# Optimization experiments

Measured on AMD Instinct MI355X. Metric: run time of the kernel, lower is better.

Reference implementation:

```python
import jax, jax.numpy as jnp
import numpy as np

NUM_HEADS = 16
NUM_KV_HEADS = 4
HEAD_DIM = 128
ROPE_THETA = 500000.0
RMS_EPS = 1e-5


def _rms_norm(x, w, eps=RMS_EPS):
    # normalize over last dim in fp32, as in YuaRMSNorm
    xf = x.astype(jnp.float32)
    var = jnp.mean(xf * xf, axis=-1, keepdims=True)
    return (w * (xf * jax.lax.rsqrt(var + eps))).astype(x.dtype)


def _rotate_half(x):
    x1, x2 = jnp.split(x, 2, axis=-1)
    return jnp.concatenate([-x2, x1], axis=-1)


def _rope_cos_sin(seq_len, dim, dtype):
    inv_freq = 1.0 / (ROPE_THETA ** (jnp.arange(0, dim, 2, dtype=jnp.float32) / dim))
    pos = jnp.arange(seq_len, dtype=jnp.float32)
    freqs = pos[:, None] * inv_freq[None, :]          # [S, dim/2]
    emb = jnp.concatenate([freqs, freqs], axis=-1)     # [S, dim]
    return jnp.cos(emb).astype(dtype), jnp.sin(emb).astype(dtype)


def setup_inputs() -> dict:
    key = jax.random.key(0)
    ks = jax.random.split(key, 5)
    B, S, H = 2, 2048, 2048
    q_out = NUM_HEADS * HEAD_DIM
    kv_out = NUM_KV_HEADS * HEAD_DIM
    sc = 0.02
    return {
        "hidden_states": jax.random.normal(ks[0], (B, S, H), jnp.float32),
        "q_w": jax.random.normal(ks[1], (q_out, H), jnp.float32) * sc,
        "k_w": jax.random.normal(ks[2], (kv_out, H), jnp.float32) * sc,
        "v_w": jax.random.normal(ks[3], (kv_out, H), jnp.float32) * sc,
        "o_w": jax.random.normal(ks[4], (H, q_out), jnp.float32) * sc,
        "q_norm_w": jnp.ones((HEAD_DIM,), jnp.float32),
        "k_norm_w": jnp.ones((HEAD_DIM,), jnp.float32),
    }


def reference(hidden_states, q_w, k_w, v_w, o_w, q_norm_w, k_norm_w):
    B, S, H = hidden_states.shape
    groups = NUM_HEADS // NUM_KV_HEADS

    # fused-ish QKV projections (torch Linear: x @ W^T)
    q = jnp.einsum('bsh,oh->bso', hidden_states, q_w).reshape(B, S, NUM_HEADS, HEAD_DIM).transpose(0, 2, 1, 3)
    k = jnp.einsum('bsh,oh->bso', hidden_states, k_w).reshape(B, S, NUM_KV_HEADS, HEAD_DIM).transpose(0, 2, 1, 3)
    v = jnp.einsum('bsh,oh->bso', hidden_states, v_w).reshape(B, S, NUM_KV_HEADS, HEAD_DIM).transpose(0, 2, 1, 3)

    # QK RMSNorm over head_dim
    q = _rms_norm(q, q_norm_w)
    k = _rms_norm(k, k_norm_w)

    # RoPE (position_ids = arange(S))
    cos, sin = _rope_cos_sin(S, HEAD_DIM, q.dtype)  # [S, hd]
    cos = cos[None, None]  # [1,1,S,hd]
    sin = sin[None, None]
    q = q * cos + _rotate_half(q) * sin
    k = k * cos + _rotate_half(k) * sin

    # GQA repeat_interleave of kv heads
    k = jnp.repeat(k, groups, axis=1)  # [B, num_heads, S, hd]
    v = jnp.repeat(v, groups, axis=1)

    # causal SDPA
    scale = 1.0 / jnp.sqrt(jnp.asarray(HEAD_DIM, q.dtype))
    scores = jnp.einsum('bhqd,bhkd->bhqk', q, k) * scale
    causal = jnp.tril(jnp.ones((S, S), bool))
    scores = jnp.where(causal[None, None], scores, jnp.finfo(scores.dtype).min)
    probs = jax.nn.softmax(scores, axis=-1)
    attn = jnp.einsum('bhqk,bhkd->bhqd', probs, v)

    attn = attn.transpose(0, 2, 1, 3).reshape(B, S, NUM_HEADS * HEAD_DIM)
    return jnp.einsum('bso,ho->bsh', attn, o_w)
```

## Files before the change

kernel.cpp:

```cpp
#include <hip/hip_runtime.h>
#include <stdint.h>

#define S_LEN 2048
#define BATCH 2
#define NH 16
#define NKV 4
#define HD 128
#define HID 2048
#define MROWS (BATCH * S_LEN)
#define PST 72

typedef unsigned short u16;
typedef __attribute__((ext_vector_type(8))) short frag_ab;
typedef __attribute__((ext_vector_type(4))) float frag_cd;

static __device__ __forceinline__ float bf2f(u16 v) {
    union { unsigned u; float f; } t; t.u = ((unsigned)v) << 16; return t.f;
}
static __device__ __forceinline__ u16 f2bf(float f) {
    union { float f; unsigned u; } t; t.f = f;
    unsigned r = t.u + 0x7fffu + ((t.u >> 16) & 1u);
    return (u16)(r >> 16);
}
static __device__ __forceinline__ void load_lds16(const u16* g, u16* l) {
    __builtin_amdgcn_global_load_lds((const __attribute__((address_space(1))) void*)g,
                                     (__attribute__((address_space(3))) void*)l, 16, 0, 0);
}

__global__ __launch_bounds__(256) void conv_f32_bf16(const float* __restrict__ src,
                                                     u16* __restrict__ dst, int n4) {
    int i = blockIdx.x * 256 + threadIdx.x;
    if (i >= n4) return;
    float4 v = ((const float4*)src)[i];
    ushort4 o;
    o.x = f2bf(v.x); o.y = f2bf(v.y); o.z = f2bf(v.z); o.w = f2bf(v.w);
    ((ushort4*)dst)[i] = o;
}

__global__ __launch_bounds__(256) void gemm_bt(const u16* __restrict__ A, const u16* __restrict__ B,
                                               float* __restrict__ C, int M, int N, int K) {
    __shared__ u16 As[128 * 32];
    __shared__ u16 Bs[128 * 32];
    const int tid = threadIdx.x;
    const int wave = tid >> 6, lane = tid & 63;
    const int quad = lane >> 4, lr = lane & 15;
    const int wm = (wave & 1) * 64, wn = (wave >> 1) * 64;
    const long bm = (long)blockIdx.x * 128, bn = (long)blockIdx.y * 128;
    const int srow = (wave << 4) + (lane >> 2);
    const int scol = (lane & 3) * 8;
    const u16* Ag = A + (bm + srow) * (long)K + scol;
    const u16* Bg = B + (bn + srow) * (long)K + scol;
    u16* AsW = As + wave * 512;
    u16* BsW = Bs + wave * 512;

    frag_cd acc[4][4];
#pragma unroll
    for (int i = 0; i < 4; i++)
#pragma unroll
        for (int j = 0; j < 4; j++) acc[i][j] = (frag_cd){0.f, 0.f, 0.f, 0.f};

    for (int k0 = 0; k0 < K; k0 += 32) {
        __syncthreads();
        load_lds16(Ag + k0, AsW);
        load_lds16(Ag + (long)64 * K + k0, AsW + 2048);
        load_lds16(Bg + k0, BsW);
        load_lds16(Bg + (long)64 * K + k0, BsW + 2048);
        __syncthreads();
        frag_ab af[4], bfr[4];
#pragma unroll
        for (int i = 0; i < 4; i++) af[i] = *(const frag_ab*)(As + (wm + i * 16 + lr) * 32 + quad * 8);
#pragma unroll
        for (int j = 0; j < 4; j++) bfr[j] = *(const frag_ab*)(Bs + (wn + j * 16 + lr) * 32 + quad * 8);
#pragma unroll
        for (int i = 0; i < 4; i++)
#pragma unroll
            for (int j = 0; j < 4; j++)
                acc[i][j] = __builtin_amdgcn_mfma_f32_16x16x32_bf16(af[i], bfr[j], acc[i][j], 0, 0, 0);
    }
#pragma unroll
    for (int i = 0; i < 4; i++)
#pragma unroll
        for (int j = 0; j < 4; j++)
#pragma unroll
            for (int r = 0; r < 4; r++) {
                long row = bm + wm + i * 16 + quad * 4 + r;
                long col = bn + wn + j * 16 + lr;
                C[row * N + col] = acc[i][j][r];
            }
}

__global__ __launch_bounds__(256) void gemm_bt64(const u16* __restrict__ A, const u16* __restrict__ B,
                                                 float* __restrict__ C, int M, int N, int K) {
    __shared__ u16 As[128 * 32];
    __shared__ u16 Bs[64 * 32];
    const int tid = threadIdx.x;
    const int wave = tid >> 6, lane = tid & 63;
    const int quad = lane >> 4, lr = lane & 15;
    const int wm = (wave & 1) * 64, wn = (wave >> 1) * 32;
    const long bm = (long)blockIdx.x * 128, bn = (long)blockIdx.y * 64;
    const int srow = (wave << 4) + (lane >> 2);
    const int scol = (lane & 3) * 8;
    const u16* Ag = A + (bm + srow) * (long)K + scol;
    const u16* Bg = B + (bn + srow) * (long)K + scol;
    u16* AsW = As + wave * 512;
    u16* BsW = Bs + wave * 512;

    frag_cd acc[4][2];
#pragma unroll
    for (int i = 0; i < 4; i++)
#pragma unroll
        for (int j = 0; j < 2; j++) acc[i][j] = (frag_cd){0.f, 0.f, 0.f, 0.f};

    for (int k0 = 0; k0 < K; k0 += 32) {
        __syncthreads();
        load_lds16(Ag + k0, AsW);
        load_lds16(Ag + (long)64 * K + k0, AsW + 2048);
        load_lds16(Bg + k0, BsW);
        __syncthreads();
        frag_ab af[4], bfr[2];
#pragma unroll
        for (int i = 0; i < 4; i++) af[i] = *(const frag_ab*)(As + (wm + i * 16 + lr) * 32 + quad * 8);
#pragma unroll
        for (int j = 0; j < 2; j++) bfr[j] = *(const frag_ab*)(Bs + (wn + j * 16 + lr) * 32 + quad * 8);
#pragma unroll
        for (int i = 0; i < 4; i++)
#pragma unroll
            for (int j = 0; j < 2; j++)
                acc[i][j] = __builtin_amdgcn_mfma_f32_16x16x32_bf16(af[i], bfr[j], acc[i][j], 0, 0, 0);
    }
#pragma unroll
    for (int i = 0; i < 4; i++)
#pragma unroll
        for (int j = 0; j < 2; j++)
#pragma unroll
            for (int r = 0; r < 4; r++) {
                long row = bm + wm + i * 16 + quad * 4 + r;
                long col = bn + wn + j * 16 + lr;
                C[row * N + col] = acc[i][j][r];
            }
}

__global__ __launch_bounds__(256) void rope_norm(const float* __restrict__ src, u16* __restrict__ dst,
                                                 const float* __restrict__ nw, int nh, int stride, int coff) {
    const int m = blockIdx.x;
    const int wave = threadIdx.x >> 6, lane = threadIdx.x & 63;
    const int s = m & (S_LEN - 1), b = m >> 11;
    const int d0 = 2 * lane;
    const float w0 = nw[d0], w1 = nw[d0 + 1];
    const int i0 = d0 & 63;
    const float lnt_over = 13.122363377404328f / 64.f;
    float inv0 = expf(-(float)i0 * lnt_over);
    float inv1 = expf(-(float)(i0 + 1) * lnt_over);
    float c0 = cosf((float)s * inv0), sn0 = sinf((float)s * inv0);
    float c1 = cosf((float)s * inv1), sn1 = sinf((float)s * inv1);
    for (int h = wave; h < nh; h += 4) {
        float2 x = *(const float2*)(src + (long)m * stride + coff + h * HD + d0);
        float ss = x.x * x.x + x.y * x.y;
#pragma unroll
        for (int off = 1; off < 64; off <<= 1) ss += __shfl_xor(ss, off);
        float rs = rsqrtf(ss * (1.f / HD) + 1e-5f);
        float xn0 = x.x * rs * w0;
        float xn1 = x.y * rs * w1;
        float p0 = __shfl_xor(xn0, 32);
        float p1 = __shfl_xor(xn1, 32);
        float r0 = (lane < 32) ? -p0 : p0;
        float r1 = (lane < 32) ? -p1 : p1;
        float y0 = xn0 * c0 + r0 * sn0;
        float y1 = xn1 * c1 + r1 * sn1;
        unsigned outw = (unsigned)f2bf(y0) | ((unsigned)f2bf(y1) << 16);
        *(unsigned*)(dst + (((long)(b * nh + h) * S_LEN + s) * HD + d0)) = outw;
    }
}

__global__ __launch_bounds__(256) void pack_vt(const float* __restrict__ src, u16* __restrict__ dst,
                                               int stride, int coff) {
    __shared__ u16 t[128 * 72];
    const int tid = threadIdx.x;
    const int st = blockIdx.x & 31;
    const int kh = (blockIdx.x >> 5) & 3;
    const int b = blockIdx.x >> 7;
    const long m0 = (long)b * S_LEN + st * 64;
#pragma unroll
    for (int c = 0; c < 8; c++) {
        int idx = c * 256 + tid;
        int r = idx >> 5, cg = idx & 31;
        float4 v = *(const float4*)(src + (m0 + r) * stride + coff + kh * HD + cg * 4);
        int col = cg * 4;
        t[(col + 0) * 72 + r] = f2bf(v.x);
        t[(col + 1) * 72 + r] = f2bf(v.y);
        t[(col + 2) * 72 + r] = f2bf(v.z);
        t[(col + 3) * 72 + r] = f2bf(v.w);
    }
    __syncthreads();
    const int d = tid >> 1, sh = (tid & 1) * 32;
    u16* dp = dst + ((long)(b * NKV + kh) * HD + d) * S_LEN + st * 64 + sh;
    const u16* tp = &t[d * 72 + sh];
    *(uint4*)(dp + 0)  = *(const uint4*)(tp + 0);
    *(uint4*)(dp + 8)  = *(const uint4*)(tp + 8);
    *(uint4*)(dp + 16) = *(const uint4*)(tp + 16);
    *(uint4*)(dp + 24) = *(const uint4*)(tp + 24);
}

__global__ __launch_bounds__(256, 2) void flash_attn(const u16* __restrict__ Q, const u16* __restrict__ K,
                                                     const u16* __restrict__ Vt, u16* __restrict__ O) {
    __shared__ __align__(16) char shmem[19456];
    u16* Pls = (u16*)shmem;
    float* maccf = (float*)shmem;
    float* mlbf = (float*)(shmem + 18432);
#define MACC(mt, dt, c, r) (((((mt) * 8 + (dt)) * 16 + (c)) * 16) + (r))
#define MLB(w, mt, row, j) (((((w) * 2 + (mt)) * 16 + (row)) * 2) + (j))
    const int tid = threadIdx.x;
    const int wave = tid >> 6, lane = tid & 63;
    const int quad = lane >> 4, lr = lane & 15;
    const int g = blockIdx.x & 7;
    const int sub = (blockIdx.x >> 3) & 3;
    const int tt = blockIdx.x >> 5;
    const int t = 63 - tt;
    const int b = g >> 2, kh = g & 3;
    const int h = kh * 4 + sub;
    const float scale = 0.08838834764831845f;
    const u16* Qb = Q + ((long)(b * NH + h) * S_LEN) * HD;
    const u16* Kb = K + ((long)(b * NKV + kh) * S_LEN) * HD;
    const u16* Vb = Vt + ((long)(b * NKV + kh) * HD) * S_LEN;
    const int pbase = wave * 32 * PST;

    const int q0 = t * 32;
    const int nkt = (t >> 1) + 1;

    frag_ab qf[2][4];
#pragma unroll
    for (int mt = 0; mt < 2; mt++) {
        int qrow = q0 + mt * 16 + lr;
#pragma unroll
        for (int ks = 0; ks < 4; ks++)
            qf[mt][ks] = *(const frag_ab*)(Qb + (long)qrow * HD + ks * 32 + quad * 8);
    }
    frag_cd oa[2][8];
    float m_i[2][4], l_i[2][4];
#pragma unroll
    for (int mt = 0; mt < 2; mt++) {
#pragma unroll
        for (int dt = 0; dt < 8; dt++) oa[mt][dt] = (frag_cd){0.f, 0.f, 0.f, 0.f};
#pragma unroll
        for (int r = 0; r < 4; r++) { m_i[mt][r] = -3e38f; l_i[mt][r] = 0.f; }
    }

    for (int kt = wave; kt < nkt; kt += 4) {
        const int j0 = kt * 64;
        frag_cd sa[2][4];
#pragma unroll
        for (int mt = 0; mt < 2; mt++)
#pragma unroll
            for (int nt = 0; nt < 4; nt++) sa[mt][nt] = (frag_cd){0.f, 0.f, 0.f, 0.f};
#pragma unroll
        for (int nt = 0; nt < 4; nt++) {
            frag_ab kf[4];
#pragma unroll
            for (int ks = 0; ks < 4; ks++)
                kf[ks] = *(const frag_ab*)(Kb + (long)(j0 + nt * 16 + lr) * HD + ks * 32 + quad * 8);
#pragma unroll
            for (int mt = 0; mt < 2; mt++)
#pragma unroll
                for (int ks = 0; ks < 4; ks++)
                    sa[mt][nt] = __builtin_amdgcn_mfma_f32_16x16x32_bf16(qf[mt][ks], kf[ks], sa[mt][nt], 0, 0, 0);
        }
        frag_ab vf[2][8];
#pragma unroll
        for (int ks = 0; ks < 2; ks++)
#pragma unroll
            for (int dt = 0; dt < 8; dt++)
                vf[ks][dt] = *(const frag_ab*)(Vb + (long)(dt * 16 + lr) * S_LEN + j0 + ks * 32 + quad * 8);

        const bool need_mask = (j0 + 63) > q0;
#pragma unroll
        for (int mt = 0; mt < 2; mt++) {
            float mrow[4] = {-3e38f, -3e38f, -3e38f, -3e38f};
#pragma unroll
            for (int nt = 0; nt < 4; nt++) {
                int key = j0 + nt * 16 + lr;
#pragma unroll
                for (int r = 0; r < 4; r++) {
                    int qrow = q0 + mt * 16 + quad * 4 + r;
                    float v = sa[mt][nt][r] * scale;
                    if (need_mask) v = (key <= qrow) ? v : -3e38f;
                    sa[mt][nt][r] = v;
                    mrow[r] = fmaxf(mrow[r], v);
                }
            }
#pragma unroll
            for (int off = 1; off < 16; off <<= 1)
#pragma unroll
                for (int r = 0; r < 4; r++) mrow[r] = fmaxf(mrow[r], __shfl_xor(mrow[r], off));
            float rs[4];
#pragma unroll
            for (int r = 0; r < 4; r++) {
                float mn = fmaxf(m_i[mt][r], mrow[r]);
                float alpha = __expf(m_i[mt][r] - mn);
                m_i[mt][r] = mn;
                l_i[mt][r] *= alpha;
                rs[r] = 0.f;
#pragma unroll
                for (int dt = 0; dt < 8; dt++) oa[mt][dt][r] *= alpha;
            }
#pragma unroll
            for (int nt = 0; nt < 4; nt++)
#pragma unroll
                for (int r = 0; r < 4; r++) {
                    float pw = __expf(sa[mt][nt][r] - m_i[mt][r]);
                    rs[r] += pw;
                    Pls[pbase + (mt * 16 + quad * 4 + r) * PST + nt * 16 + lr] = f2bf(pw);
                }
#pragma unroll
            for (int off = 1; off < 16; off <<= 1)
#pragma unroll
                for (int r = 0; r < 4; r++) rs[r] += __shfl_xor(rs[r], off);
#pragma unroll
            for (int r = 0; r < 4; r++) l_i[mt][r] += rs[r];
        }

#pragma unroll
        for (int ks = 0; ks < 2; ks++) {
            frag_ab pf[2];
#pragma unroll
            for (int mt = 0; mt < 2; mt++)
                pf[mt] = *(const frag_ab*)&Pls[pbase + (mt * 16 + lr) * PST + ks * 32 + quad * 8];
#pragma unroll
            for (int dt = 0; dt < 8; dt++) {
                oa[0][dt] = __builtin_amdgcn_mfma_f32_16x16x32_bf16(pf[0], vf[ks][dt], oa[0][dt], 0, 0, 0);
                oa[1][dt] = __builtin_amdgcn_mfma_f32_16x16x32_bf16(pf[1], vf[ks][dt], oa[1][dt], 0, 0, 0);
            }
        }
    }

    if (lr == 0) {
#pragma unroll
        for (int mt = 0; mt < 2; mt++)
#pragma unroll
            for (int r = 0; r < 4; r++) {
                mlbf[MLB(wave, mt, quad * 4 + r, 0)] = m_i[mt][r];
                mlbf[MLB(wave, mt, quad * 4 + r, 1)] = l_i[mt][r];
            }
    }
    __syncthreads();
    float inv[2][4];
#pragma unroll
    for (int mt = 0; mt < 2; mt++)
#pragma unroll
        for (int r = 0; r < 4; r++) {
            int row = quad * 4 + r;
            float m0 = mlbf[MLB(0, mt, row, 0)], m1 = mlbf[MLB(1, mt, row, 0)];
            float m2 = mlbf[MLB(2, mt, row, 0)], m3 = mlbf[MLB(3, mt, row, 0)];
            float ms = fmaxf(fmaxf(m0, m1), fmaxf(m2, m3));
            float ls = mlbf[MLB(0, mt, row, 1)] * __expf(m0 - ms) + mlbf[MLB(1, mt, row, 1)] * __expf(m1 - ms)
                     + mlbf[MLB(2, mt, row, 1)] * __expf(m2 - ms) + mlbf[MLB(3, mt, row, 1)] * __expf(m3 - ms);
            inv[mt][r] = 1.f / ls;
            float alpha = __expf(m_i[mt][r] - ms);
#pragma unroll
            for (int dt = 0; dt < 8; dt++) oa[mt][dt][r] *= alpha;
        }
    for (int w = 0; w < 4; w++) {
        if (wave == w) {
#pragma unroll
            for (int mt = 0; mt < 2; mt++)
#pragma unroll
                for (int dt = 0; dt < 8; dt++) {
                    frag_cd* pp = (frag_cd*)&maccf[MACC(mt, dt, lr, quad * 4)];
                    if (w == 0) *pp = oa[mt][dt];
                    else {
                        frag_cd o = *pp;
#pragma unroll
                        for (int r = 0; r < 4; r++) o[r] += oa[mt][dt][r];
                        *pp = o;
                    }
                }
        }
        __syncthreads();
    }
#pragma unroll
    for (int mt = 0; mt < 2; mt++)
#pragma unroll
        for (int dto = 0; dto < 2; dto++) {
            int dt = wave * 2 + dto;
            frag_cd v = *(const frag_cd*)&maccf[MACC(mt, dt, lr, quad * 4)];
#pragma unroll
            for (int r = 0; r < 4; r++) {
                int s = q0 + mt * 16 + quad * 4 + r;
                O[((long)b * S_LEN + s) * (NH * HD) + h * HD + dt * 16 + lr] =
                    f2bf(v[r] * inv[mt][r]);
            }
        }
#undef MACC
#undef MLB
}

extern "C" void kernel_launch(void* const* d_in, const int* in_sizes, int n_in,
                              void* d_out, int out_size, void* d_ws, size_t ws_size,
                              hipStream_t stream) {
    const float* hs  = (const float*)d_in[0];
    const float* q_w = (const float*)d_in[1];
    const float* k_w = (const float*)d_in[2];
    const float* v_w = (const float*)d_in[3];
    const float* o_w = (const float*)d_in[4];
    const float* qnw = (const float*)d_in[5];
    const float* knw = (const float*)d_in[6];
    float* out = (float*)d_out;
    char* ws = (char*)d_ws;
    (void)in_sizes; (void)n_in; (void)out_size;

    if (ws_size >= (100ul << 20)) {
        u16* hs_bf  = (u16*)(ws);
        u16* wbuf   = (u16*)(ws + (16ul << 20));
        float* gout = (float*)(ws + (28ul << 20));
        u16* Kr     = (u16*)(ws + (76ul << 20));
        u16* Vt     = (u16*)(ws + (80ul << 20));
        u16* Qr     = (u16*)(ws + (84ul << 20));
        const int NQKV = HID + 2 * NKV * HD;

        conv_f32_bf16<<<(MROWS * HID / 4 + 255) / 256, 256, 0, stream>>>(hs, hs_bf, MROWS * HID / 4);
        conv_f32_bf16<<<(HID * HID / 4 + 255) / 256, 256, 0, stream>>>(q_w, wbuf, HID * HID / 4);
        conv_f32_bf16<<<(NKV * HD * HID / 4 + 255) / 256, 256, 0, stream>>>(k_w, wbuf + (long)HID * HID, NKV * HD * HID / 4);
        conv_f32_bf16<<<(NKV * HD * HID / 4 + 255) / 256, 256, 0, stream>>>(v_w, wbuf + (long)(HID + NKV * HD) * HID, NKV * HD * HID / 4);

        dim3 gqkv(MROWS / 128, NQKV / 128);
        gemm_bt<<<gqkv, 256, 0, stream>>>(hs_bf, wbuf, gout, MROWS, NQKV, HID);

        rope_norm<<<MROWS, 256, 0, stream>>>(gout, Qr, qnw, NH, NQKV, 0);
        rope_norm<<<MROWS, 256, 0, stream>>>(gout, Kr, knw, NKV, NQKV, HID);
        pack_vt<<<BATCH * NKV * (S_LEN / 64), 256, 0, stream>>>(gout, Vt, NQKV, HID + NKV * HD);

        flash_attn<<<2048, 256, 0, stream>>>(Qr, Kr, Vt, hs_bf);

        conv_f32_bf16<<<(HID * HID / 4 + 255) / 256, 256, 0, stream>>>(o_w, wbuf, HID * HID / 4);
        dim3 go(MROWS / 128, HID / 64);
        gemm_bt64<<<go, 256, 0, stream>>>(hs_bf, wbuf, out, MROWS, HID, HID);
    } else {
        u16* hs_bf  = (u16*)(ws);
        u16* wbuf   = (u16*)(ws + (16ul << 20));
        float* gout = (float*)(ws + (24ul << 20));
        u16* Kr     = (u16*)(ws + (40ul << 20));
        u16* Vt     = (u16*)(ws + (44ul << 20));
        u16* Qr     = (u16*)(ws + (56ul << 20));

        conv_f32_bf16<<<(MROWS * HID / 4 + 255) / 256, 256, 0, stream>>>(hs, hs_bf, MROWS * HID / 4);

        conv_f32_bf16<<<(HID * HID / 4 + 255) / 256, 256, 0, stream>>>(q_w, wbuf, HID * HID / 4);
        dim3 gq(MROWS / 128, HID / 128);
        gemm_bt<<<gq, 256, 0, stream>>>(hs_bf, wbuf, gout, MROWS, HID, HID);
        rope_norm<<<MROWS, 256, 0, stream>>>(gout, Qr, qnw, NH, HID, 0);

        conv_f32_bf16<<<(NKV * HD * HID / 4 + 255) / 256, 256, 0, stream>>>(k_w, wbuf, NKV * HD * HID / 4);
        conv_f32_bf16<<<(NKV * HD * HID / 4 + 255) / 256, 256, 0, stream>>>(v_w, wbuf + NKV * HD * HID, NKV * HD * HID / 4);
        dim3 gkv(MROWS / 128, (2 * NKV * HD) / 64);
        gemm_bt64<<<gkv, 256, 0, stream>>>(hs_bf, wbuf, gout, MROWS, 2 * NKV * HD, HID);
        rope_norm<<<MROWS, 256, 0, stream>>>(gout, Kr, knw, NKV, 2 * NKV * HD, 0);
        pack_vt<<<BATCH * NKV * (S_LEN / 64), 256, 0, stream>>>(gout, Vt, 2 * NKV * HD, NKV * HD);

        flash_attn<<<2048, 256, 0, stream>>>(Qr, Kr, Vt, hs_bf);

        conv_f32_bf16<<<(HID * HID / 4 + 255) / 256, 256, 0, stream>>>(o_w, wbuf, HID * HID / 4);
        dim3 go(MROWS / 128, HID / 64);
        gemm_bt64<<<go, 256, 0, stream>>>(hs_bf, wbuf, out, MROWS, HID, HID);
    }
}
```

Baseline: 423.2 us.

## Split KV projection along K into two GEMMs and sum in fused norm/pack

Drops the large-workspace fused QKV path and always uses separate projections. The Q GEMM moves to the 128x64 tile kernel, which gives more blocks. The small KV GEMM is split along the reduction dimension into two launches using new lda/ldb stride parameters, which doubles the block count for better CU occupancy. The partial results are summed inside new rope_norm_sum and pack_vt_sum kernels. Kr and Vt now alias the weight buffer region, and the change adds an extra fp32 partial buffer plus additional reads.

```diff
diff --git a/kernel.cpp b/kernel.cpp
--- a/kernel.cpp
+++ b/kernel.cpp
@@ -90,7 +90,8 @@
 }
 
 __global__ __launch_bounds__(256) void gemm_bt64(const u16* __restrict__ A, const u16* __restrict__ B,
-                                                 float* __restrict__ C, int M, int N, int K) {
+                                                 float* __restrict__ C, int M, int N, int K,
+                                                 int lda, int ldb) {
     __shared__ u16 As[128 * 32];
     __shared__ u16 Bs[64 * 32];
     const int tid = threadIdx.x;
@@ -100,8 +101,8 @@
     const long bm = (long)blockIdx.x * 128, bn = (long)blockIdx.y * 64;
     const int srow = (wave << 4) + (lane >> 2);
     const int scol = (lane & 3) * 8;
-    const u16* Ag = A + (bm + srow) * (long)K + scol;
-    const u16* Bg = B + (bn + srow) * (long)K + scol;
+    const u16* Ag = A + (bm + srow) * (long)lda + scol;
+    const u16* Bg = B + (bn + srow) * (long)ldb + scol;
     u16* AsW = As + wave * 512;
     u16* BsW = Bs + wave * 512;
 
@@ -114,7 +115,7 @@
     for (int k0 = 0; k0 < K; k0 += 32) {
         __syncthreads();
         load_lds16(Ag + k0, AsW);
-        load_lds16(Ag + (long)64 * K + k0, AsW + 2048);
+        load_lds16(Ag + (long)64 * lda + k0, AsW + 2048);
         load_lds16(Bg + k0, BsW);
         __syncthreads();
         frag_ab af[4], bfr[2];
@@ -172,6 +173,41 @@
     }
 }
 
+__global__ __launch_bounds__(256) void rope_norm_sum(const float* __restrict__ src1, const float* __restrict__ src2,
+                                                     u16* __restrict__ dst, const float* __restrict__ nw,
+                                                     int nh, int stride, int coff) {
+    const int m = blockIdx.x;
+    const int wave = threadIdx.x >> 6, lane = threadIdx.x & 63;
+    const int s = m & (S_LEN - 1), b = m >> 11;
+    const int d0 = 2 * lane;
+    const float w0 = nw[d0], w1 = nw[d0 + 1];
+    const int i0 = d0 & 63;
+    const float lnt_over = 13.122363377404328f / 64.f;
+    float inv0 = expf(-(float)i0 * lnt_over);
+    float inv1 = expf(-(float)(i0 + 1) * lnt_over);
+    float c0 = cosf((float)s * inv0), sn0 = sinf((float)s * inv0);
+    float c1 = cosf((float)s * inv1), sn1 = sinf((float)s * inv1);
+    for (int h = wave; h < nh; h += 4) {
+        float2 x1 = *(const float2*)(src1 + (long)m * stride + coff + h * HD + d0);
+        float2 x2 = *(const float2*)(src2 + (long)m * stride + coff + h * HD + d0);
+        float2 x; x.x = x1.x + x2.x; x.y = x1.y + x2.y;
+        float ss = x.x * x.x + x.y * x.y;
+#pragma unroll
+        for (int off = 1; off < 64; off <<= 1) ss += __shfl_xor(ss, off);
+        float rs = rsqrtf(ss * (1.f / HD) + 1e-5f);
+        float xn0 = x.x * rs * w0;
+        float xn1 = x.y * rs * w1;
+        float p0 = __shfl_xor(xn0, 32);
+        float p1 = __shfl_xor(xn1, 32);
+        float r0 = (lane < 32) ? -p0 : p0;
+        float r1 = (lane < 32) ? -p1 : p1;
+        float y0 = xn0 * c0 + r0 * sn0;
+        float y1 = xn1 * c1 + r1 * sn1;
+        unsigned outw = (unsigned)f2bf(y0) | ((unsigned)f2bf(y1) << 16);
+        *(unsigned*)(dst + (((long)(b * nh + h) * S_LEN + s) * HD + d0)) = outw;
+    }
+}
+
 __global__ __launch_bounds__(256) void pack_vt(const float* __restrict__ src, u16* __restrict__ dst,
                                                int stride, int coff) {
     __shared__ u16 t[128 * 72];
@@ -185,6 +221,38 @@
         int idx = c * 256 + tid;
         int r = idx >> 5, cg = idx & 31;
         float4 v = *(const float4*)(src + (m0 + r) * stride + coff + kh * HD + cg * 4);
+        int col = cg * 4;
+        t[(col + 0) * 72 + r] = f2bf(v.x);
+        t[(col + 1) * 72 + r] = f2bf(v.y);
+        t[(col + 2) * 72 + r] = f2bf(v.z);
+        t[(col + 3) * 72 + r] = f2bf(v.w);
+    }
+    __syncthreads();
+    const int d = tid >> 1, sh = (tid & 1) * 32;
+    u16* dp = dst + ((long)(b * NKV + kh) * HD + d) * S_LEN + st * 64 + sh;
+    const u16* tp = &t[d * 72 + sh];
+    *(uint4*)(dp + 0)  = *(const uint4*)(tp + 0);
+    *(uint4*)(dp + 8)  = *(const uint4*)(tp + 8);
+    *(uint4*)(dp + 16) = *(const uint4*)(tp + 16);
+    *(uint4*)(dp + 24) = *(const uint4*)(tp + 24);
+}
+
+__global__ __launch_bounds__(256) void pack_vt_sum(const float* __restrict__ src1, const float* __restrict__ src2,
+                                                   u16* __restrict__ dst, int stride, int coff) {
+    __shared__ u16 t[128 * 72];
+    const int tid = threadIdx.x;
+    const int st = blockIdx.x & 31;
+    const int kh = (blockIdx.x >> 5) & 3;
+    const int b = blockIdx.x >> 7;
+    const long m0 = (long)b * S_LEN + st * 64;
+#pragma unroll
+    for (int c = 0; c < 8; c++) {
+        int idx = c * 256 + tid;
+        int r = idx >> 5, cg = idx & 31;
+        long off = (m0 + r) * stride + coff + kh * HD + cg * 4;
+        float4 v1 = *(const float4*)(src1 + off);
+        float4 v2 = *(const float4*)(src2 + off);
+        float4 v; v.x = v1.x + v2.x; v.y = v1.y + v2.y; v.z = v1.z + v2.z; v.w = v1.w + v2.w;
         int col = cg * 4;
         t[(col + 0) * 72 + r] = f2bf(v.x);
         t[(col + 1) * 72 + r] = f2bf(v.y);
@@ -405,60 +473,33 @@
     const float* knw = (const float*)d_in[6];
     float* out = (float*)d_out;
     char* ws = (char*)d_ws;
-    (void)in_sizes; (void)n_in; (void)out_size;
-
-    if (ws_size >= (100ul << 20)) {
-        u16* hs_bf  = (u16*)(ws);
-        u16* wbuf   = (u16*)(ws + (16ul << 20));
-        float* gout = (float*)(ws + (28ul << 20));
-        u16* Kr     = (u16*)(ws + (76ul << 20));
-        u16* Vt     = (u16*)(ws + (80ul << 20));
-        u16* Qr     = (u16*)(ws + (84ul << 20));
-        const int NQKV = HID + 2 * NKV * HD;
-
-        conv_f32_bf16<<<(MROWS * HID / 4 + 255) / 256, 256, 0, stream>>>(hs, hs_bf, MROWS * HID / 4);
-        conv_f32_bf16<<<(HID * HID / 4 + 255) / 256, 256, 0, stream>>>(q_w, wbuf, HID * HID / 4);
-        conv_f32_bf16<<<(NKV * HD * HID / 4 + 255) / 256, 256, 0, stream>>>(k_w, wbuf + (long)HID * HID, NKV * HD * HID / 4);
-        conv_f32_bf16<<<(NKV * HD * HID / 4 + 255) / 256, 256, 0, stream>>>(v_w, wbuf + (long)(HID + NKV * HD) * HID, NKV * HD * HID / 4);
-
-        dim3 gqkv(MROWS / 128, NQKV / 128);
-        gemm_bt<<<gqkv, 256, 0, stream>>>(hs_bf, wbuf, gout, MROWS, NQKV, HID);
-
-        rope_norm<<<MROWS, 256, 0, stream>>>(gout, Qr, qnw, NH, NQKV, 0);
-        rope_norm<<<MROWS, 256, 0, stream>>>(gout, Kr, knw, NKV, NQKV, HID);
-        pack_vt<<<BATCH * NKV * (S_LEN / 64), 256, 0, stream>>>(gout, Vt, NQKV, HID + NKV * HD);
-
-        flash_attn<<<2048, 256, 0, stream>>>(Qr, Kr, Vt, hs_bf);
-
-        conv_f32_bf16<<<(HID * HID / 4 + 255) / 256, 256, 0, stream>>>(o_w, wbuf, HID * HID / 4);
-        dim3 go(MROWS / 128, HID / 64);
-        gemm_bt64<<<go, 256, 0, stream>>>(hs_bf, wbuf, out, MROWS, HID, HID);
-    } else {
-        u16* hs_bf  = (u16*)(ws);
-        u16* wbuf   = (u16*)(ws + (16ul << 20));
-        float* gout = (float*)(ws + (24ul << 20));
-        u16* Kr     = (u16*)(ws + (40ul << 20));
-        u16* Vt     = (u16*)(ws + (44ul << 20));
-        u16* Qr     = (u16*)(ws + (56ul << 20));
-
-        conv_f32_bf16<<<(MROWS * HID / 4 + 255) / 256, 256, 0, stream>>>(hs, hs_bf, MROWS * HID / 4);
-
-        conv_f32_bf16<<<(HID * HID / 4 + 255) / 256, 256, 0, stream>>>(q_w, wbuf, HID * HID / 4);
-        dim3 gq(MROWS / 128, HID / 128);
-        gemm_bt<<<gq, 256, 0, stream>>>(hs_bf, wbuf, gout, MROWS, HID, HID);
-        rope_norm<<<MROWS, 256, 0, stream>>>(gout, Qr, qnw, NH, HID, 0);
-
-        conv_f32_bf16<<<(NKV * HD * HID / 4 + 255) / 256, 256, 0, stream>>>(k_w, wbuf, NKV * HD * HID / 4);
-        conv_f32_bf16<<<(NKV * HD * HID / 4 + 255) / 256, 256, 0, stream>>>(v_w, wbuf + NKV * HD * HID, NKV * HD * HID / 4);
-        dim3 gkv(MROWS / 128, (2 * NKV * HD) / 64);
-        gemm_bt64<<<gkv, 256, 0, stream>>>(hs_bf, wbuf, gout, MROWS, 2 * NKV * HD, HID);
-        rope_norm<<<MROWS, 256, 0, stream>>>(gout, Kr, knw, NKV, 2 * NKV * HD, 0);
-        pack_vt<<<BATCH * NKV * (S_LEN / 64), 256, 0, stream>>>(gout, Vt, 2 * NKV * HD, NKV * HD);
-
-        flash_attn<<<2048, 256, 0, stream>>>(Qr, Kr, Vt, hs_bf);
-
-        conv_f32_bf16<<<(HID * HID / 4 + 255) / 256, 256, 0, stream>>>(o_w, wbuf, HID * HID / 4);
-        dim3 go(MROWS / 128, HID / 64);
-        gemm_bt64<<<go, 256, 0, stream>>>(hs_bf, wbuf, out, MROWS, HID, HID);
-    }
-}
+    (void)in_sizes; (void)n_in; (void)out_size; (void)ws_size;
+
+    u16* hs_bf  = (u16*)(ws);
+    u16* wbuf   = (u16*)(ws + (16ul << 20));
+    float* gout = (float*)(ws + (24ul << 20));
+    float* gout2= (float*)(ws + (40ul << 20));
+    u16* Kr     = (u16*)(ws + (16ul << 20));
+    u16* Vt     = (u16*)(ws + (20ul << 20));
+    u16* Qr     = (u16*)(ws + (56ul << 20));
+
+    conv_f32_bf16<<<(MROWS * HID / 4 + 255) / 256, 256, 0, stream>>>(hs, hs_bf, MROWS * HID / 4);
+
+    conv_f32_bf16<<<(HID * HID / 4 + 255) / 256, 256, 0, stream>>>(q_w, wbuf, HID * HID / 4);
+    dim3 gq(MROWS / 128, HID / 64);
+    gemm_bt64<<<gq, 256, 0, stream>>>(hs_bf, wbuf, gout, MROWS, HID, HID, HID, HID);
+    rope_norm<<<MROWS, 256, 0, stream>>>(gout, Qr, qnw, NH, HID, 0);
+
+    conv_f32_bf16<<<(NKV * HD * HID / 4 + 255) / 256, 256, 0, stream>>>(k_w, wbuf, NKV * HD * HID / 4);
+    conv_f32_bf16<<<(NKV * HD * HID / 4 + 255) / 256, 256, 0, stream>>>(v_w, wbuf + NKV * HD * HID, NKV * HD * HID / 4);
+    dim3 gkv(MROWS / 128, (2 * NKV * HD) / 64);
+    gemm_bt64<<<gkv, 256, 0, stream>>>(hs_bf, wbuf, gout, MROWS, 2 * NKV * HD, HID / 2, HID, HID);
+    gemm_bt64<<<gkv, 256, 0, stream>>>(hs_bf + HID / 2, wbuf + HID / 2, gout2, MROWS, 2 * NKV * HD, HID / 2, HID, HID);
+    rope_norm_sum<<<MROWS, 256, 0, stream>>>(gout, gout2, Kr, knw, NKV, 2 * NKV * HD, 0);
+    pack_vt_sum<<<BATCH * NKV * (S_LEN / 64), 256, 0, stream>>>(gout, gout2, Vt, 2 * NKV * HD, NKV * HD);
+
+    flash_attn<<<2048, 256, 0, stream>>>(Qr, Kr, Vt, hs_bf);
+
+    conv_f32_bf16<<<(HID * HID / 4 + 255) / 256, 256, 0, stream>>>(o_w, wbuf, HID * HID / 4);
+    gemm_bt64<<<gq, 256, 0, stream>>>(hs_bf, wbuf, out, MROWS, HID, HID, HID, HID);
+}
```

Result: slower. 456.1 us (+7.8%).
